# Kernel tuning notes

Hardware: AMD Instinct MI355X
Metric: run time of the kernel (lower is better)

## Reference

```python
import jax, jax.numpy as jnp
import numpy as np

N = 100000   # nodes
E = 1600000  # edges (avg degree 16)
D = 64       # in_channels
OUT = 64     # out_channels


def setup_inputs() -> dict:
    key = jax.random.key(0)
    k1, k2, k3, k4, k5 = jax.random.split(key, 5)
    x = jax.random.normal(k1, (N, D), jnp.float32)
    edge_index = jax.random.randint(k2, (2, E), 0, N, dtype=jnp.int32)
    x0 = jax.random.normal(k3, (N, D), jnp.float32)
    W_weight = jax.random.normal(k4, (OUT, D), jnp.float32) * (1.0 / np.sqrt(D))
    W_bias = jax.random.normal(k5, (OUT,), jnp.float32) * 0.01
    return {"x": x, "edge_index": edge_index, "x0": x0,
            "W_weight": W_weight, "W_bias": W_bias}


def reference(x, edge_index, x0, W_bias, W_weight):
    n = x.shape[0]
    # gcn_norm with add_self_loops=True (PyG default), improved=False
    self_loops = jnp.arange(n, dtype=edge_index.dtype)
    row = jnp.concatenate([edge_index[0], self_loops])  # source nodes
    col = jnp.concatenate([edge_index[1], self_loops])  # target nodes
    w = jnp.ones(row.shape[0], dtype=x.dtype)
    deg = jax.ops.segment_sum(w, col, num_segments=n)   # in-degree (+1 self loop)
    deg_inv_sqrt = jnp.where(deg > 0, jax.lax.rsqrt(jnp.maximum(deg, 1e-12)), 0.0)
    norm = deg_inv_sqrt[row] * deg_inv_sqrt[col]        # [E+N]
    # SpMM: adj_t = SparseTensor(row=col, col=row) -> out[c] = sum_e norm_e * x[row_e]
    agg = jax.ops.segment_sum(x[row] * norm[:, None], col, num_segments=n)  # [N, D]
    # use_init=False, use_weight=True -> trailing Linear
    return agg @ W_weight.T + W_bias
```

## Files before the change

kernel.cpp:

```cpp
#include <hip/hip_runtime.h>


#define NBMAX 400
#define CAP   5120

typedef short bf16x8 __attribute__((ext_vector_type(8)));
typedef float f32x4  __attribute__((ext_vector_type(4)));

__device__ inline float bflo(unsigned u) { return __uint_as_float(u << 16); }
__device__ inline float bfhi(unsigned u) { return __uint_as_float(u & 0xFFFF0000u); }
__device__ inline unsigned short f2bf(float f) {
    unsigned u = __float_as_uint(f);
    u += 0x7FFFu + ((u >> 16) & 1u);
    return (unsigned short)(u >> 16);
}

__global__ void k_initcur(int* __restrict__ gcur, int NB) {
    int b = threadIdx.x;
    if (b < NB) gcur[b] = b * CAP;
}

__global__ __launch_bounds__(512) void k_bin(const int* __restrict__ row,
                                             const int* __restrict__ col,
                                             int* __restrict__ gcur,
                                             unsigned int* __restrict__ ebuf, int E) {
    __shared__ unsigned int   sorted4[4096];
    __shared__ unsigned short sbkt[4096];
    __shared__ int h[NBMAX], hstart[NBMAX], hcur[NBMAX], gof[NBMAX];
    int t = threadIdx.x;
    int base = blockIdx.x * 4096;
    int total = min(4096, E - base);

    int rr[8], cc[8];
    #pragma unroll
    for (int i = 0; i < 2; ++i) {
        int e0 = (t + i * 512) * 4;
        if (e0 + 3 < total) {
            int4 r4 = *(const int4*)(row + base + e0);
            int4 c4 = *(const int4*)(col + base + e0);
            rr[i*4+0]=r4.x; rr[i*4+1]=r4.y; rr[i*4+2]=r4.z; rr[i*4+3]=r4.w;
            cc[i*4+0]=c4.x; cc[i*4+1]=c4.y; cc[i*4+2]=c4.z; cc[i*4+3]=c4.w;
        } else {
            #pragma unroll
            for (int j = 0; j < 4; ++j) {
                int e = e0 + j;
                if (e < total) { rr[i*4+j] = row[base+e]; cc[i*4+j] = col[base+e]; }
                else cc[i*4+j] = -1;
            }
        }
    }
    for (int b = t; b < NBMAX; b += 512) h[b] = 0;
    __syncthreads();
    #pragma unroll
    for (int i = 0; i < 8; ++i)
        if (cc[i] >= 0) atomicAdd(&h[cc[i] >> 8], 1);
    __syncthreads();
    if (t < 64) {
        int lo = t * 7;
        int loc[7]; int s = 0;
        #pragma unroll
        for (int i = 0; i < 7; ++i) {
            loc[i] = s;
            int idx = lo + i;
            s += (idx < NBMAX) ? h[idx] : 0;
        }
        int incl = s;
        for (int off = 1; off < 64; off <<= 1) {
            int v = __shfl_up(incl, off);
            if (t >= off) incl += v;
        }
        int ex = incl - s;
        #pragma unroll
        for (int i = 0; i < 7; ++i) {
            int idx = lo + i;
            if (idx < NBMAX) hstart[idx] = ex + loc[i];
        }
    }
    __syncthreads();
    for (int b = t; b < NBMAX; b += 512) hcur[b] = hstart[b];
    __syncthreads();
    #pragma unroll
    for (int i = 0; i < 8; ++i) {
        if (cc[i] >= 0) {
            int b = cc[i] >> 8;
            int rank = atomicAdd(&hcur[b], 1);
            sorted4[rank] = (unsigned)rr[i] | ((unsigned)(cc[i] & 255) << 24);
            sbkt[rank] = (unsigned short)b;
        }
    }
    for (int b = t; b < NBMAX; b += 512) {
        int m = h[b];
        gof[b] = m ? atomicAdd(&gcur[b], m) : 0;
    }
    __syncthreads();
    for (int i = t; i < total; i += 512) {
        int b = sbkt[i];
        ebuf[gof[b] + (i - hstart[b])] = sorted4[i];
    }
}

__global__ __launch_bounds__(256) void k_cnt(const unsigned int* __restrict__ ebuf,
                                             const int* __restrict__ gcur,
                                             float* __restrict__ dinv, int n) {
    __shared__ int h[256];
    int b = blockIdx.x, t = threadIdx.x;
    int s0 = b * CAP;
    int count = min(gcur[b] - s0, CAP);
    h[t] = 0;
    __syncthreads();
    for (int i = t; i < count; i += 256) atomicAdd(&h[ebuf[s0 + i] >> 24], 1);
    __syncthreads();
    int c = b * 256 + t;
    if (c < n) dinv[c] = rsqrtf((float)(h[t] + 1));
}

__global__ __launch_bounds__(256) void k_gemm(const float* __restrict__ x,
                                              const float* __restrict__ W,
                                              const float* __restrict__ dinv,
                                              unsigned short* __restrict__ yb, int n) {
    __shared__ __align__(16) unsigned short xs[64][72];
    __shared__ __align__(16) unsigned short Wb[64][72];
    int t = threadIdx.x;
    long long total = (long long)n * 64;
    long long xbase = (long long)blockIdx.x * 4096;
    #pragma unroll
    for (int i = 0; i < 4; ++i) {
        int idx = t + i * 256;
        int r = idx >> 4, c4 = (idx & 15) << 2;
        long long g = xbase + (long long)idx * 4;
        float4 v;
        if (g + 3 < total) v = *(const float4*)(x + g);
        else {
            v.x = (g + 0 < total) ? x[g + 0] : 0.f;
            v.y = (g + 1 < total) ? x[g + 1] : 0.f;
            v.z = (g + 2 < total) ? x[g + 2] : 0.f;
            v.w = (g + 3 < total) ? x[g + 3] : 0.f;
        }
        ushort4 o; o.x = f2bf(v.x); o.y = f2bf(v.y); o.z = f2bf(v.z); o.w = f2bf(v.w);
        *(ushort4*)&xs[r][c4] = o;
        float4 wv = *(const float4*)(W + idx * 4);
        ushort4 wo; wo.x = f2bf(wv.x); wo.y = f2bf(wv.y); wo.z = f2bf(wv.z); wo.w = f2bf(wv.w);
        *(ushort4*)&Wb[r][c4] = wo;
    }
    __syncthreads();
    int lane = t & 63, wid = t >> 6;
    int m  = wid * 16 + (lane & 15);
    int kg = (lane >> 4) * 8;
    bf16x8 a0 = *(bf16x8*)&xs[m][kg];
    bf16x8 a1 = *(bf16x8*)&xs[m][32 + kg];
    int bn = lane & 15;
    f32x4 acc0 = {0.f,0.f,0.f,0.f}, acc1 = acc0, acc2 = acc0, acc3 = acc0;
    {
        bf16x8 b0 = *(bf16x8*)&Wb[bn][kg], b1 = *(bf16x8*)&Wb[bn][32 + kg];
        acc0 = __builtin_amdgcn_mfma_f32_16x16x32_bf16(a0, b0, acc0, 0, 0, 0);
        acc0 = __builtin_amdgcn_mfma_f32_16x16x32_bf16(a1, b1, acc0, 0, 0, 0);
    }
    {
        bf16x8 b0 = *(bf16x8*)&Wb[bn + 16][kg], b1 = *(bf16x8*)&Wb[bn + 16][32 + kg];
        acc1 = __builtin_amdgcn_mfma_f32_16x16x32_bf16(a0, b0, acc1, 0, 0, 0);
        acc1 = __builtin_amdgcn_mfma_f32_16x16x32_bf16(a1, b1, acc1, 0, 0, 0);
    }
    {
        bf16x8 b0 = *(bf16x8*)&Wb[bn + 32][kg], b1 = *(bf16x8*)&Wb[bn + 32][32 + kg];
        acc2 = __builtin_amdgcn_mfma_f32_16x16x32_bf16(a0, b0, acc2, 0, 0, 0);
        acc2 = __builtin_amdgcn_mfma_f32_16x16x32_bf16(a1, b1, acc2, 0, 0, 0);
    }
    {
        bf16x8 b0 = *(bf16x8*)&Wb[bn + 48][kg], b1 = *(bf16x8*)&Wb[bn + 48][32 + kg];
        acc3 = __builtin_amdgcn_mfma_f32_16x16x32_bf16(a0, b0, acc3, 0, 0, 0);
        acc3 = __builtin_amdgcn_mfma_f32_16x16x32_bf16(a1, b1, acc3, 0, 0, 0);
    }
    int rbase = blockIdx.x * 64 + wid * 16 + (lane >> 4) * 4;
    #pragma unroll
    for (int i = 0; i < 4; ++i) {
        int r = rbase + i;
        if (r < n) {
            float dv = dinv[r];
            long long ro = (long long)r * 64 + (lane & 15);
            yb[ro +  0] = f2bf(dv * acc0[i]);
            yb[ro + 16] = f2bf(dv * acc1[i]);
            yb[ro + 32] = f2bf(dv * acc2[i]);
            yb[ro + 48] = f2bf(dv * acc3[i]);
        }
    }
}

__global__ __launch_bounds__(1024) void k_aggr(const unsigned int* __restrict__ ebuf,
                                               const int* __restrict__ gcur,
                                               const float* __restrict__ dinv,
                                               const unsigned short* __restrict__ yb,
                                               const float* __restrict__ bias,
                                               float* __restrict__ out, int n) {
    __shared__ int h[256], hstart[256], hc[256], wsum[4];
    __shared__ int sbuf[CAP];
    int b = blockIdx.x, t = threadIdx.x;
    int s0 = b * CAP;
    int count = min(gcur[b] - s0, CAP);

    if (t < 256) h[t] = 0;
    __syncthreads();
    unsigned rec[5];
    #pragma unroll
    for (int k = 0; k < 5; ++k) {
        int i = t + k * 1024;
        if (i < count) {
            unsigned p = ebuf[s0 + i];
            rec[k] = p;
            atomicAdd(&h[p >> 24], 1);
        }
    }
    __syncthreads();
    if (t < 256) {
        int v = h[t];
        int lane = t & 63, wid = t >> 6;
        int incl = v;
        #pragma unroll
        for (int off = 1; off < 64; off <<= 1) {
            int u = __shfl_up(incl, off);
            if (lane >= off) incl += u;
        }
        hstart[t] = incl;
        if (lane == 63) wsum[wid] = incl;
    }
    __syncthreads();
    if (t < 256) {
        int wid = t >> 6;
        int add = 0;
        for (int w = 0; w < wid; ++w) add += wsum[w];
        int ex = hstart[t] - h[t] + add;
        hstart[t] = ex;
        hc[t] = ex;
    }
    __syncthreads();
    #pragma unroll
    for (int k = 0; k < 5; ++k) {
        int i = t + k * 1024;
        if (i < count) {
            unsigned p = rec[k];
            int r = atomicAdd(&hc[p >> 24], 1);
            sbuf[r] = (int)(p & 0x1FFFFu);
        }
    }
    __syncthreads();

    int lane = t & 63, w = t >> 6;
    int g = lane >> 4, q = lane & 15;
    #pragma unroll
    for (int r = 0; r < 4; ++r) {
        int cl = r * 64 + w * 4 + g;
        int c = b * 256 + cl;
        if (c >= n) continue;
        int start = hstart[cl], len = h[cl];
        float a0 = 0.f, a1 = 0.f, a2 = 0.f, a3 = 0.f;
        if (len > 0) {
            int sc = sbuf[start];
            for (int i = 0; i < len; ++i) {
                int sn = (i + 1 < len) ? sbuf[start + i + 1] : 0;
                float2 v = *(const float2*)(yb + (long long)sc * 64 + (q << 2));
                unsigned u0 = __float_as_uint(v.x), u1 = __float_as_uint(v.y);
                a0 += bflo(u0); a1 += bfhi(u0);
                a2 += bflo(u1); a3 += bfhi(u1);
                sc = sn;
            }
        }
        {
            float2 v = *(const float2*)(yb + (long long)c * 64 + (q << 2));
            unsigned u0 = __float_as_uint(v.x), u1 = __float_as_uint(v.y);
            a0 += bflo(u0); a1 += bfhi(u0);
            a2 += bflo(u1); a3 += bfhi(u1);
        }
        float dc = dinv[c];
        float4 bv = *(const float4*)(bias + (q << 2));
        *(float4*)(out + (long long)c * 64 + (q << 2)) =
            make_float4(dc * a0 + bv.x, dc * a1 + bv.y,
                        dc * a2 + bv.z, dc * a3 + bv.w);
    }
}

extern "C" void kernel_launch(void* const* d_in, const int* in_sizes, int n_in,
                              void* d_out, int out_size, void* d_ws, size_t ws_size,
                              hipStream_t stream) {
    const float* x    = (const float*)d_in[0];
    const int*   ei   = (const int*)d_in[1];
    const float* W    = (const float*)d_in[3];
    const float* bias = (const float*)d_in[4];
    float* out = (float*)d_out;

    int n = in_sizes[0] / 64;
    int E = in_sizes[1] / 2;
    const int* row = ei;
    const int* col = ei + E;

    int NB = (n + 255) / 256;

    char* ws = (char*)d_ws;
    size_t off = 0;
    auto alloc = [&](size_t bytes) { char* p = ws + off; off += (bytes + 15) & ~size_t(15); return p; };
    int*            gcur = (int*)  alloc((size_t)NB * 4);
    float*          dinv = (float*)alloc((size_t)n * 4);
    unsigned short* yb   = (unsigned short*)alloc((size_t)n * 64 * 2);
    unsigned int*   ebuf = (unsigned int*)alloc((size_t)NB * CAP * 4);

    int nbE = (E + 4095) / 4096;

    k_initcur<<<1, 512, 0, stream>>>(gcur, NB);
    k_bin <<<nbE, 512, 0, stream>>>(row, col, gcur, ebuf, E);
    k_cnt <<<NB, 256, 0, stream>>>(ebuf, gcur, dinv, n);
    k_gemm<<<(n + 63) / 64, 256, 0, stream>>>(x, W, dinv, yb, n);
    k_aggr<<<NB, 1024, 0, stream>>>(ebuf, gcur, dinv, yb, bias, out, n);
}
```

Baseline: 177.1 us.

## Fuse degree counting into GEMM kernel and derive dinv locally in aggregation

Removes the separate degree-count kernel and the dinv buffer. The GEMM kernel now builds each 64-row block's in-degree histogram by scanning its bucket's edge records, and the aggregation kernel recomputes the normalisation from the per-node edge count it already has. A memset replaces the cursor-init kernel, and bucket offsets are now added at bin time. The cost is that each bucket's edges are read four times by GEMM blocks and filtered, adding redundant loads in exchange for fewer launches and less global traffic for dinv.

```diff
diff --git a/kernel.cpp b/kernel.cpp
--- a/kernel.cpp
+++ b/kernel.cpp
@@ -15,14 +15,9 @@
     return (unsigned short)(u >> 16);
 }
 
-__global__ void k_initcur(int* __restrict__ gcur, int NB) {
-    int b = threadIdx.x;
-    if (b < NB) gcur[b] = b * CAP;
-}
-
 __global__ __launch_bounds__(512) void k_bin(const int* __restrict__ row,
                                              const int* __restrict__ col,
-                                             int* __restrict__ gcur,
+                                             int* __restrict__ gcnt,
                                              unsigned int* __restrict__ ebuf, int E) {
     __shared__ unsigned int   sorted4[4096];
     __shared__ unsigned short sbkt[4096];
@@ -90,7 +85,7 @@
     }
     for (int b = t; b < NBMAX; b += 512) {
         int m = h[b];
-        gof[b] = m ? atomicAdd(&gcur[b], m) : 0;
+        gof[b] = b * CAP + (m ? atomicAdd(&gcnt[b], m) : 0);
     }
     __syncthreads();
     for (int i = t; i < total; i += 512) {
@@ -99,30 +94,18 @@
     }
 }
 
-__global__ __launch_bounds__(256) void k_cnt(const unsigned int* __restrict__ ebuf,
-                                             const int* __restrict__ gcur,
-                                             float* __restrict__ dinv, int n) {
-    __shared__ int h[256];
-    int b = blockIdx.x, t = threadIdx.x;
-    int s0 = b * CAP;
-    int count = min(gcur[b] - s0, CAP);
-    h[t] = 0;
-    __syncthreads();
-    for (int i = t; i < count; i += 256) atomicAdd(&h[ebuf[s0 + i] >> 24], 1);
-    __syncthreads();
-    int c = b * 256 + t;
-    if (c < n) dinv[c] = rsqrtf((float)(h[t] + 1));
-}
-
-__global__ __launch_bounds__(256) void k_gemm(const float* __restrict__ x,
-                                              const float* __restrict__ W,
-                                              const float* __restrict__ dinv,
-                                              unsigned short* __restrict__ yb, int n) {
+__global__ __launch_bounds__(256) void k_gemmcnt(const float* __restrict__ x,
+                                                 const float* __restrict__ W,
+                                                 const unsigned int* __restrict__ ebuf,
+                                                 const int* __restrict__ gcnt,
+                                                 unsigned short* __restrict__ yb, int n) {
     __shared__ __align__(16) unsigned short xs[64][72];
     __shared__ __align__(16) unsigned short Wb[64][72];
+    __shared__ int hd[64];
     int t = threadIdx.x;
     long long total = (long long)n * 64;
     long long xbase = (long long)blockIdx.x * 4096;
+    if (t < 64) hd[t] = 0;
     #pragma unroll
     for (int i = 0; i < 4; ++i) {
         int idx = t + i * 256;
@@ -142,6 +125,16 @@
         ushort4 wo; wo.x = f2bf(wv.x); wo.y = f2bf(wv.y); wo.z = f2bf(wv.z); wo.w = f2bf(wv.w);
         *(ushort4*)&Wb[r][c4] = wo;
     }
+    {
+        int bb  = blockIdx.x >> 2;
+        int sub = blockIdx.x & 3;
+        int s0 = bb * CAP;
+        int count = min(gcnt[bb], CAP);
+        for (int i = t; i < count; i += 256) {
+            unsigned d = ebuf[s0 + i] >> 24;
+            if ((int)(d >> 6) == sub) atomicAdd(&hd[d & 63], 1);
+        }
+    }
     __syncthreads();
     int lane = t & 63, wid = t >> 6;
     int m  = wid * 16 + (lane & 15);
@@ -170,13 +163,14 @@
         acc3 = __builtin_amdgcn_mfma_f32_16x16x32_bf16(a0, b0, acc3, 0, 0, 0);
         acc3 = __builtin_amdgcn_mfma_f32_16x16x32_bf16(a1, b1, acc3, 0, 0, 0);
     }
-    int rbase = blockIdx.x * 64 + wid * 16 + (lane >> 4) * 4;
+    int lr0 = wid * 16 + (lane >> 4) * 4;
+    int rbase = blockIdx.x * 64 + lr0;
     #pragma unroll
     for (int i = 0; i < 4; ++i) {
         int r = rbase + i;
         if (r < n) {
-            float dv = dinv[r];
-            long long ro = (long long)r * 64 + (lane & 15);
+            float dv = rsqrtf((float)hd[lr0 + i] + 1.0f);
+            long long ro = (long long)r * 64 + bn;
             yb[ro +  0] = f2bf(dv * acc0[i]);
             yb[ro + 16] = f2bf(dv * acc1[i]);
             yb[ro + 32] = f2bf(dv * acc2[i]);
@@ -186,8 +180,7 @@
 }
 
 __global__ __launch_bounds__(1024) void k_aggr(const unsigned int* __restrict__ ebuf,
-                                               const int* __restrict__ gcur,
-                                               const float* __restrict__ dinv,
+                                               const int* __restrict__ gcnt,
                                                const unsigned short* __restrict__ yb,
                                                const float* __restrict__ bias,
                                                float* __restrict__ out, int n) {
@@ -195,7 +188,7 @@
     __shared__ int sbuf[CAP];
     int b = blockIdx.x, t = threadIdx.x;
     int s0 = b * CAP;
-    int count = min(gcur[b] - s0, CAP);
+    int count = min(gcnt[b], CAP);
 
     if (t < 256) h[t] = 0;
     __syncthreads();
@@ -269,7 +262,7 @@
             a0 += bflo(u0); a1 += bfhi(u0);
             a2 += bflo(u1); a3 += bfhi(u1);
         }
-        float dc = dinv[c];
+        float dc = rsqrtf((float)len + 1.0f);
         float4 bv = *(const float4*)(bias + (q << 2));
         *(float4*)(out + (long long)c * 64 + (q << 2)) =
             make_float4(dc * a0 + bv.x, dc * a1 + bv.y,
@@ -296,16 +289,14 @@
     char* ws = (char*)d_ws;
     size_t off = 0;
     auto alloc = [&](size_t bytes) { char* p = ws + off; off += (bytes + 15) & ~size_t(15); return p; };
-    int*            gcur = (int*)  alloc((size_t)NB * 4);
-    float*          dinv = (float*)alloc((size_t)n * 4);
+    int*            gcnt = (int*)  alloc((size_t)NB * 4);
     unsigned short* yb   = (unsigned short*)alloc((size_t)n * 64 * 2);
     unsigned int*   ebuf = (unsigned int*)alloc((size_t)NB * CAP * 4);
 
     int nbE = (E + 4095) / 4096;
 
-    k_initcur<<<1, 512, 0, stream>>>(gcur, NB);
-    k_bin <<<nbE, 512, 0, stream>>>(row, col, gcur, ebuf, E);
-    k_cnt <<<NB, 256, 0, stream>>>(ebuf, gcur, dinv, n);
-    k_gemm<<<(n + 63) / 64, 256, 0, stream>>>(x, W, dinv, yb, n);
-    k_aggr<<<NB, 1024, 0, stream>>>(ebuf, gcur, dinv, yb, bias, out, n);
-}
+    hipMemsetAsync(gcnt, 0, (size_t)NB * 4, stream);
+    k_bin    <<<nbE, 512, 0, stream>>>(row, col, gcnt, ebuf, E);
+    k_gemmcnt<<<(n + 63) / 64, 256, 0, stream>>>(x, W, ebuf, gcnt, yb, n);
+    k_aggr   <<<NB, 1024, 0, stream>>>(ebuf, gcnt, yb, bias, out, n);
+}
```

After: 176.0 us. About the same (-0.6%).
